# Kernel tuning notes

Hardware: AMD Instinct MI355X
Metric: run time of the kernel (lower is better)

## Reference

```python
import jax, jax.numpy as jnp
import numpy as np

N_EMBD = 1024
N_HEAD = 16
LORA_R = 8
LORA_ALPHA = 16
SCALE = LORA_ALPHA / LORA_R


def lora_linear(x, W, b, A, Bm):
    # loralib: F.linear(x, W, b) + (x @ A.T @ B.T) * scaling
    return x @ W.T + b + ((x @ A.T) @ Bm.T) * SCALE


def setup_inputs() -> dict:
    key = jax.random.key(0)
    ks = jax.random.split(key, 9)
    B, T, C = 4, 2048, N_EMBD
    s_in = 1.0 / np.sqrt(C)
    x = jax.random.normal(ks[0], (B, T, C), dtype=jnp.float32)
    Wqkv = jax.random.normal(ks[1], (3 * C, C), dtype=jnp.float32) * s_in
    bqkv = jnp.zeros((3 * C,), dtype=jnp.float32)
    Aqkv = jax.random.normal(ks[2], (LORA_R, C), dtype=jnp.float32) * s_in
    Bqkv = jnp.zeros((3 * C, LORA_R), dtype=jnp.float32)  # loralib inits B to zero
    Wproj = jax.random.normal(ks[3], (C, C), dtype=jnp.float32) * s_in
    bproj = jnp.zeros((C,), dtype=jnp.float32)
    Aproj = jax.random.normal(ks[4], (LORA_R, C), dtype=jnp.float32) * s_in
    Bproj = jnp.zeros((C, LORA_R), dtype=jnp.float32)
    return {"x": x, "Wqkv": Wqkv, "bqkv": bqkv, "Aqkv": Aqkv, "Bqkv": Bqkv,
            "Wproj": Wproj, "bproj": bproj, "Aproj": Aproj, "Bproj": Bproj}


def reference(x, Wqkv, bqkv, Aqkv, Bqkv, Wproj, bproj, Aproj, Bproj):
    B, T, C = x.shape
    H, D = N_HEAD, C // N_HEAD
    qkv = lora_linear(x, Wqkv, bqkv, Aqkv, Bqkv)  # [B,T,3C]
    q, k, v = jnp.split(qkv, 3, axis=2)
    # [B,T,C] -> [B,H,T,D]
    q = q.reshape(B, T, H, D).transpose(0, 2, 1, 3)
    k = k.reshape(B, T, H, D).transpose(0, 2, 1, 3)
    v = v.reshape(B, T, H, D).transpose(0, 2, 1, 3)
    att = jnp.einsum("bhqd,bhkd->bhqk", q, k) * (1.0 / np.sqrt(D))
    causal = jnp.tril(jnp.ones((T, T), dtype=bool))
    att = jnp.where(causal[None, None], att, jnp.float32(-jnp.inf))
    att = jax.nn.softmax(att, axis=-1)
    out = jnp.einsum("bhqk,bhkd->bhqd", att, v)  # [B,H,T,D]
    out = out.transpose(0, 2, 1, 3).reshape(B, T, C)
    return lora_linear(out, Wproj, bproj, Aproj, Bproj)
```

## Files before the change

### kernel.cpp

```cpp
#include <hip/hip_runtime.h>
#include <hip/hip_bf16.h>

typedef __bf16 bf16_t;
typedef __bf16 bf16x8 __attribute__((ext_vector_type(8)));
typedef __bf16 bf16x4 __attribute__((ext_vector_type(4)));
typedef float  f32x4  __attribute__((ext_vector_type(4)));

#define MFMA_BF16 __builtin_amdgcn_mfma_f32_16x16x32_bf16
#define NEG_BIG  (-3.0e38f)

#if __has_builtin(__builtin_amdgcn_exp2f)
#define EXP2F(x) __builtin_amdgcn_exp2f(x)
#else
#define EXP2F(x) exp2f(x)
#endif

#define SBAR()       __builtin_amdgcn_s_barrier()
#define SCHED0()     __builtin_amdgcn_sched_barrier(0)
#define WAIT_LGKM0() asm volatile("s_waitcnt lgkmcnt(0)" ::: "memory")
#define WAIT_LGKM8() asm volatile("s_waitcnt lgkmcnt(8)" ::: "memory")
#define WAIT_VM0()   asm volatile("s_waitcnt vmcnt(0)" ::: "memory")
#define WAIT_VM4()   asm volatile("s_waitcnt vmcnt(4)" ::: "memory")
#define WAIT_VM6()   asm volatile("s_waitcnt vmcnt(6)" ::: "memory")

__device__ __forceinline__ void load16_lds(const bf16_t* g, bf16_t* l) {
    __builtin_amdgcn_global_load_lds(
        (const __attribute__((address_space(1))) void*)g,
        (__attribute__((address_space(3))) void*)l, 16, 0, 0);
}

__device__ inline bf16x8 ld8(const bf16_t* p) { return *(const bf16x8*)p; }
__device__ inline bf16x8 ld8(const float* p) {
    f32x4 a = *(const f32x4*)p;
    f32x4 b = *(const f32x4*)(p + 4);
    bf16x8 o;
    o[0] = (bf16_t)a[0]; o[1] = (bf16_t)a[1]; o[2] = (bf16_t)a[2]; o[3] = (bf16_t)a[3];
    o[4] = (bf16_t)b[0]; o[5] = (bf16_t)b[1]; o[6] = (bf16_t)b[2]; o[7] = (bf16_t)b[3];
    return o;
}

template <typename TX>
__device__ __forceinline__ void lora_xa_body(
    const TX* __restrict__ X, const float* __restrict__ A,
    float* __restrict__ out, int m, int lane)
{
    const TX* xp = X + (size_t)m * 1024;
    float acc[8];
#pragma unroll
    for (int r = 0; r < 8; r++) acc[r] = 0.f;

#pragma unroll 4
    for (int ci = 0; ci < 16; ci++) {
        int k = ci * 64 + lane;
        float xv = (float)xp[k];
#pragma unroll
        for (int r = 0; r < 8; r++) acc[r] += xv * A[r * 1024 + k];
    }
#pragma unroll
    for (int r = 0; r < 8; r++) {
        float v = acc[r];
        v += __shfl_xor(v, 1);  v += __shfl_xor(v, 2);  v += __shfl_xor(v, 4);
        v += __shfl_xor(v, 8);  v += __shfl_xor(v, 16); v += __shfl_xor(v, 32);
        if (lane == 0) out[m * 8 + r] = v;
    }
}

template <typename TX>
__global__ __launch_bounds__(256) void lora_xa_kernel(
    const TX* __restrict__ X, const float* __restrict__ A,
    float* __restrict__ out)
{
    const int lane = threadIdx.x & 63;
    const int w    = threadIdx.x >> 6;
    const int m    = blockIdx.x * 4 + w;
    lora_xa_body<TX>(X, A, out, m, lane);
}

__global__ __launch_bounds__(256) void prep_kernel(
    const float* __restrict__ x, const float* __restrict__ Wqkv,
    const float* __restrict__ Wproj,
    bf16_t* __restrict__ x16, bf16_t* __restrict__ Wqkv16,
    bf16_t* __restrict__ Wproj16,
    const float* __restrict__ Aqkv, float* __restrict__ xa1)
{
    const int bid = blockIdx.x;
    if (bid < 6144) {
        const float* in; bf16_t* out; size_t off;
        if (bid < 4096)      { in = x;     out = x16;     off = (size_t)bid * 2048; }
        else if (bid < 5632) { in = Wqkv;  out = Wqkv16;  off = (size_t)(bid - 4096) * 2048; }
        else                 { in = Wproj; out = Wproj16; off = (size_t)(bid - 5632) * 2048; }
        size_t i = off + (size_t)threadIdx.x * 8;
        *(bf16x8*)&out[i] = ld8(&in[i]);
    } else {
        const int lane = threadIdx.x & 63;
        const int w    = threadIdx.x >> 6;
        const int m    = (bid - 6144) * 4 + w;
        lora_xa_body<float>(x, Aqkv, xa1, m, lane);
    }
}

__device__ __forceinline__ void gemm_epilogue(
    f32x4 (&acc)[4][4], const float* bias, const float* xA, const float* LB,
    bf16_t* C0, bf16_t* C1, bf16_t* C2, float* Cf,
    int tile_m, int tile_n, int wm, int wn, int c, int g)
{
    const int seg    = tile_n >> 10;
    const int tn_loc = tile_n & 1023;
    bf16_t* Cout = (seg == 0) ? C0 : (seg == 1) ? C1 : C2;

    float biasf[4];
    float lbv[4][8];
#pragma unroll
    for (int j = 0; j < 4; j++) {
        int col = tile_n + wn + j * 16 + c;
        biasf[j] = bias[col];
        f32x4 lb0 = *(const f32x4*)&LB[(size_t)col * 8];
        f32x4 lb1 = *(const f32x4*)&LB[(size_t)col * 8 + 4];
#pragma unroll
        for (int r = 0; r < 4; r++) { lbv[j][r] = lb0[r]; lbv[j][r + 4] = lb1[r]; }
    }
#pragma unroll
    for (int i = 0; i < 4; i++) {
#pragma unroll
        for (int rg = 0; rg < 4; rg++) {
            int row = tile_m + wm + i * 16 + g * 4 + rg;
            f32x4 xa0 = *(const f32x4*)&xA[(size_t)row * 8];
            f32x4 xa1 = *(const f32x4*)&xA[(size_t)row * 8 + 4];
#pragma unroll
            for (int j = 0; j < 4; j++) {
                float lora = xa0[0] * lbv[j][0] + xa0[1] * lbv[j][1] +
                             xa0[2] * lbv[j][2] + xa0[3] * lbv[j][3] +
                             xa1[0] * lbv[j][4] + xa1[1] * lbv[j][5] +
                             xa1[2] * lbv[j][6] + xa1[3] * lbv[j][7];
                float v = acc[i][j][rg] + biasf[j] + 2.0f * lora;
                int lcol = tn_loc + wn + j * 16 + c;
                if (Cf) Cf[(size_t)row * 1024 + lcol] = v;
                else    Cout[(size_t)row * 1024 + lcol] = (bf16_t)v;
            }
        }
    }
}

template <typename TA, typename TW>
__global__ __launch_bounds__(256) void gemm_bias_lora(
    const TA* __restrict__ A, const TW* __restrict__ W,
    const float* __restrict__ bias, const float* __restrict__ xA,
    const float* __restrict__ LB,
    bf16_t* __restrict__ C0, bf16_t* __restrict__ C1, bf16_t* __restrict__ C2,
    float* __restrict__ Cf, int K)
{
    __shared__ __align__(16) bf16_t As[128 * 72];
    __shared__ __align__(16) bf16_t Bs[128 * 72];

    const int t    = threadIdx.x;
    const int lane = t & 63;
    const int w    = t >> 6;
    const int wm   = (w >> 1) * 64;
    const int wn   = (w & 1) * 64;
    const int c    = lane & 15;
    const int g    = lane >> 4;
    const int tile_m = blockIdx.y * 128;
    const int tile_n = blockIdx.x * 128;

    const int srow = t >> 3;
    const int scol = (t & 7) * 8;

    f32x4 acc[4][4];
#pragma unroll
    for (int i = 0; i < 4; i++)
#pragma unroll
        for (int j = 0; j < 4; j++) {
            f32x4 z = {0.f, 0.f, 0.f, 0.f};
            acc[i][j] = z;
        }

    for (int k0 = 0; k0 < K; k0 += 64) {
#pragma unroll
        for (int i = 0; i < 4; i++) {
            int r = srow + i * 32;
            *(bf16x8*)&As[r * 72 + scol] = ld8(&A[(size_t)(tile_m + r) * K + k0 + scol]);
            *(bf16x8*)&Bs[r * 72 + scol] = ld8(&W[(size_t)(tile_n + r) * K + k0 + scol]);
        }
        __syncthreads();

#pragma unroll
        for (int kk = 0; kk < 2; kk++) {
            bf16x8 af[4], bfr[4];
#pragma unroll
            for (int i = 0; i < 4; i++)
                af[i] = *(const bf16x8*)&As[(wm + i * 16 + c) * 72 + kk * 32 + g * 8];
#pragma unroll
            for (int j = 0; j < 4; j++)
                bfr[j] = *(const bf16x8*)&Bs[(wn + j * 16 + c) * 72 + kk * 32 + g * 8];
#pragma unroll
            for (int i = 0; i < 4; i++)
#pragma unroll
                for (int j = 0; j < 4; j++)
                    acc[i][j] = MFMA_BF16(af[i], bfr[j], acc[i][j], 0, 0, 0);
        }
        __syncthreads();
    }
    gemm_epilogue(acc, bias, xA, LB, C0, C1, C2, Cf, tile_m, tile_n, wm, wn, c, g);
}

#define AS_OFF(row, q) ((row) * 64 + (((q) ^ ((row) & 7)) * 8))

__global__ __launch_bounds__(256) void gemm_async(
    const bf16_t* __restrict__ A, const bf16_t* __restrict__ W,
    const float* __restrict__ bias, const float* __restrict__ xA,
    const float* __restrict__ LB,
    bf16_t* __restrict__ C0, bf16_t* __restrict__ C1, bf16_t* __restrict__ C2,
    float* __restrict__ Cf, int K)
{
    __shared__ __align__(16) bf16_t As[128 * 64];
    __shared__ __align__(16) bf16_t Bs[128 * 64];

    const int t    = threadIdx.x;
    const int lane = t & 63;
    const int w    = t >> 6;
    const int wm   = (w >> 1) * 64;
    const int wn   = (w & 1) * 64;
    const int c    = lane & 15;
    const int g    = lane >> 4;
    const int tile_m = blockIdx.y * 128;
    const int tile_n = blockIdx.x * 128;

    const int trow = t >> 3;
    const int k8   = (t & 7) ^ (trow & 7);
    const bf16_t* Ab = A + (size_t)tile_m * K + k8 * 8;
    const bf16_t* Wb = W + (size_t)tile_n * K + k8 * 8;

    f32x4 acc[4][4];
#pragma unroll
    for (int i = 0; i < 4; i++)
#pragma unroll
        for (int j = 0; j < 4; j++) {
            f32x4 z = {0.f, 0.f, 0.f, 0.f};
            acc[i][j] = z;
        }

    for (int k0 = 0; k0 < K; k0 += 64) {
#pragma unroll
        for (int i = 0; i < 4; i++) {
            int row = i * 32 + trow;
            load16_lds(&Ab[(size_t)row * K + k0], &As[(i * 256 + t) * 8]);
            load16_lds(&Wb[(size_t)row * K + k0], &Bs[(i * 256 + t) * 8]);
        }
        __syncthreads();

#pragma unroll
        for (int kk = 0; kk < 2; kk++) {
            bf16x8 af[4], bfr[4];
#pragma unroll
            for (int i = 0; i < 4; i++)
                af[i] = *(const bf16x8*)&As[AS_OFF(wm + i * 16 + c, kk * 4 + g)];
#pragma unroll
            for (int j = 0; j < 4; j++)
                bfr[j] = *(const bf16x8*)&Bs[AS_OFF(wn + j * 16 + c, kk * 4 + g)];
#pragma unroll
            for (int i = 0; i < 4; i++)
#pragma unroll
                for (int j = 0; j < 4; j++)
                    acc[i][j] = MFMA_BF16(af[i], bfr[j], acc[i][j], 0, 0, 0);
        }
        __syncthreads();
    }
    gemm_epilogue(acc, bias, xA, LB, C0, C1, C2, Cf, tile_m, tile_n, wm, wn, c, g);
}

__global__ __launch_bounds__(512, 2) void gemm_256(
    const bf16_t* __restrict__ A, const bf16_t* __restrict__ W,
    const float* __restrict__ bias, const float* __restrict__ xA,
    const float* __restrict__ LB,
    bf16_t* __restrict__ C0, bf16_t* __restrict__ C1, bf16_t* __restrict__ C2,
    float* __restrict__ Cf, int K, int ntn)
{
    __shared__ __align__(16) bf16_t As[4][8192];
    __shared__ __align__(16) bf16_t Bs[4][8192];

    const int t    = threadIdx.x;
    const int lane = t & 63;
    const int w    = t >> 6;
    const int c    = lane & 15;
    const int g    = lane >> 4;

    const int nwg = gridDim.x;
    const int cpx = nwg >> 3;
    const int bid = blockIdx.x;
    const int swz = (bid & 7) * cpx + (bid >> 3);
    const int tile_m = (swz / ntn) * 256;
    const int tile_n = (swz % ntn) * 256;

    const int wm  = (w >> 2) * 128;
    const int wn  = (w & 3) * 64;
    const int ha  = w >> 2;
    const int hb  = wn >> 7;
    const int wnl = wn & 127;

    int aoffs[8][2], boffs[4][2];
#pragma unroll
    for (int il = 0; il < 8; il++) {
        int rl = il * 16 + c;
#pragma unroll
        for (int ks = 0; ks < 2; ks++)
            aoffs[il][ks] = rl * 64 + (((ks * 4 + g) ^ (rl & 7)) * 8);
    }
#pragma unroll
    for (int j2 = 0; j2 < 4; j2++) {
        int rl = wnl + j2 * 16 + c;
#pragma unroll
        for (int ks = 0; ks < 2; ks++)
            boffs[j2][ks] = rl * 64 + (((ks * 4 + g) ^ (rl & 7)) * 8);
    }

    const int trow = t >> 3;
    const int qq   = (t & 7) ^ (trow & 7);
    const bf16_t* aO = A + (size_t)(tile_m + trow) * K + qq * 8;
    const bf16_t* wO = W + (size_t)(tile_n + trow) * K + qq * 8;
    const size_t rK64 = (size_t)64 * K;

#define STAGE_A(T, h) do {                                                         \
    load16_lds(aO + (size_t)(h) * 128 * K + (size_t)(T) * 64,                      \
               &As[((T) & 1) * 2 + (h)][t * 8]);                                   \
    load16_lds(aO + (size_t)(h) * 128 * K + rK64 + (size_t)(T) * 64,               \
               &As[((T) & 1) * 2 + (h)][4096 + t * 8]); } while (0)
#define STAGE_B(T, h) do {                                                         \
    load16_lds(wO + (size_t)(h) * 128 * K + (size_t)(T) * 64,                      \
               &Bs[((T) & 1) * 2 + (h)][t * 8]);                                   \
    load16_lds(wO + (size_t)(h) * 128 * K + rK64 + (size_t)(T) * 64,               \
               &Bs[((T) & 1) * 2 + (h)][4096 + t * 8]); } while (0)

    f32x4 acc[8][4];
#pragma unroll
    for (int i = 0; i < 8; i++)
#pragma unroll
        for (int j2 = 0; j2 < 4; j2++) {
            f32x4 z = {0.f, 0.f, 0.f, 0.f};
            acc[i][j2] = z;
        }

    const int NT = K >> 6;

    STAGE_B(0, 0); STAGE_B(0, 1); STAGE_A(0, 0); STAGE_A(0, 1);
    WAIT_VM4();
    STAGE_B(1, 0); STAGE_B(1, 1); STAGE_A(1, 0);
    WAIT_VM6();
    SBAR();

    for (int j = 0; j < NT; j++) {
        const bf16_t* Ab = &As[(j & 1) * 2 + ha][0];
        const bf16_t* Bb = &Bs[(j & 1) * 2 + hb][0];
        bf16x8 bfr[4][2], af0[4], af1[4];

#pragma unroll
        for (int j2 = 0; j2 < 4; j2++) {
            bfr[j2][0] = *(const bf16x8*)&Bb[boffs[j2][0]];
            bfr[j2][1] = *(const bf16x8*)&Bb[boffs[j2][1]];
        }
#pragma unroll
        for (int i = 0; i < 4; i++) af0[i] = *(const bf16x8*)&Ab[aoffs[i][0]];
        if (j + 1 < NT) STAGE_A(j + 1, 1);
        WAIT_LGKM8();
        SBAR();
        WAIT_LGKM0();
        SCHED0();
        __builtin_amdgcn_s_setprio(1);
#pragma unroll
        for (int i = 0; i < 4; i++)
#pragma unroll
            for (int j2 = 0; j2 < 4; j2++)
                acc[i][j2] = MFMA_BF16(af0[i], bfr[j2][0], acc[i][j2], 0, 0, 0);
        __builtin_amdgcn_s_setprio(0);
        SBAR();

#pragma unroll
        for (int i = 0; i < 4; i++) af1[i] = *(const bf16x8*)&Ab[aoffs[i + 4][0]];
        if (j + 2 < NT) STAGE_B(j + 2, 0);
        SBAR();
        WAIT_LGKM0();
        SCHED0();
        __builtin_amdgcn_s_setprio(1);
#pragma unroll
        for (int i = 0; i < 4; i++)
#pragma unroll
            for (int j2 = 0; j2 < 4; j2++)
                acc[4 + i][j2] = MFMA_BF16(af1[i], bfr[j2][0], acc[4 + i][j2], 0, 0, 0);
        __builtin_amdgcn_s_setprio(0);
        SBAR();

#pragma unroll
        for (int i = 0; i < 4; i++) af0[i] = *(const bf16x8*)&Ab[aoffs[i][1]];
#pragma unroll
        for (int i = 0; i < 4; i++) af1[i] = *(const bf16x8*)&Ab[aoffs[i + 4][1]];
        if (j + 2 < NT) STAGE_B(j + 2, 1);
        SBAR();
        WAIT_LGKM0();
        SCHED0();
        __builtin_amdgcn_s_setprio(1);
#pragma unroll
        for (int i = 0; i < 4; i++)
#pragma unroll
            for (int j2 = 0; j2 < 4; j2++)
                acc[i][j2] = MFMA_BF16(af0[i], bfr[j2][1], acc[i][j2], 0, 0, 0);
        __builtin_amdgcn_s_setprio(0);
        SBAR();

        if (j + 2 < NT) STAGE_A(j + 2, 0);
        SBAR();
        __builtin_amdgcn_s_setprio(1);
#pragma unroll
        for (int i = 0; i < 4; i++)
#pragma unroll
            for (int j2 = 0; j2 < 4; j2++)
                acc[4 + i][j2] = MFMA_BF16(af1[i], bfr[j2][1], acc[4 + i][j2], 0, 0, 0);
        __builtin_amdgcn_s_setprio(0);
        if (j < NT - 2) WAIT_VM6(); else WAIT_VM0();
        SBAR();
    }
#undef STAGE_A
#undef STAGE_B

    const int seg    = tile_n >> 10;
    const int tn_loc = tile_n & 1023;
    bf16_t* Cout = (seg == 0) ? C0 : (seg == 1) ? C1 : C2;

    float biasf[4];
    float lbv[4][8];
#pragma unroll
    for (int j2 = 0; j2 < 4; j2++) {
        int col = tile_n + wn + j2 * 16 + c;
        biasf[j2] = bias[col];
        f32x4 lb0 = *(const f32x4*)&LB[(size_t)col * 8];
        f32x4 lb1 = *(const f32x4*)&LB[(size_t)col * 8 + 4];
#pragma unroll
        for (int r = 0; r < 4; r++) { lbv[j2][r] = lb0[r]; lbv[j2][r + 4] = lb1[r]; }
    }
#pragma unroll
    for (int i = 0; i < 8; i++) {
#pragma unroll
        for (int rg = 0; rg < 4; rg++) {
            int row = tile_m + wm + i * 16 + g * 4 + rg;
            f32x4 xa0 = *(const f32x4*)&xA[(size_t)row * 8];
            f32x4 xa1 = *(const f32x4*)&xA[(size_t)row * 8 + 4];
#pragma unroll
            for (int j2 = 0; j2 < 4; j2++) {
                float lora = xa0[0] * lbv[j2][0] + xa0[1] * lbv[j2][1] +
                             xa0[2] * lbv[j2][2] + xa0[3] * lbv[j2][3] +
                             xa1[0] * lbv[j2][4] + xa1[1] * lbv[j2][5] +
                             xa1[2] * lbv[j2][6] + xa1[3] * lbv[j2][7];
                float v = acc[i][j2][rg] + biasf[j2] + 2.0f * lora;
                int lcol = tn_loc + wn + j2 * 16 + c;
                if (Cf) Cf[(size_t)row * 1024 + lcol] = v;
                else    Cout[(size_t)row * 1024 + lcol] = (bf16_t)v;
            }
        }
    }
}

#define VT_IDX(d, kv) ((d) * 72 + ((d) >> 4) * 16 + (kv))
#define PS_IDX(q, kv) ((q) * 72 + ((q) >> 2) * 8 + (kv))
#define PW_REGION 1168

__global__ __launch_bounds__(256, 2) void attn_kernel(
    bf16_t* __restrict__ Q, const bf16_t* __restrict__ Kg,
    const bf16_t* __restrict__ Vg)
{
    __shared__ __align__(16) bf16_t Ks[64 * 72];
    __shared__ __align__(16) bf16_t Vt[64 * 72 + 64];
    __shared__ __align__(16) bf16_t Ps[8 * PW_REGION];

    const int t    = threadIdx.x;
    const int lane = t & 63;
    const int w    = t >> 6;
    const int c    = lane & 15;
    const int g    = lane >> 4;

    const int id = blockIdx.x;
    const int qb = 15 - (id >> 6);
    const int h  = id & 15;
    const int b  = (id >> 4) & 3;
    const int q0 = qb * 128;
    const size_t base = (size_t)b * 2048 * 1024;
    const int last = 2 * qb + 1;

    bf16x8 qfA[2], qfB[2];
    {
        const bf16_t* qpA = Q + base + (size_t)(q0 + w * 16 + c) * 1024 + h * 64;
        qfA[0] = *(const bf16x8*)&qpA[g * 8];
        qfA[1] = *(const bf16x8*)&qpA[32 + g * 8];
        const bf16_t* qpB = qpA + (size_t)64 * 1024;
        qfB[0] = *(const bf16x8*)&qpB[g * 8];
        qfB[1] = *(const bf16x8*)&qpB[32 + g * 8];
    }

    bf16x8 ones;
#pragma unroll
    for (int e = 0; e < 8; e++) ones[e] = (bf16_t)1.0f;

    f32x4 accA[4], accB[4];
#pragma unroll
    for (int jd = 0; jd < 4; jd++) {
        f32x4 z = {0.f, 0.f, 0.f, 0.f};
        accA[jd] = z; accB[jd] = z;
    }
    f32x4 lA = {0.f, 0.f, 0.f, 0.f};
    f32x4 lB = {0.f, 0.f, 0.f, 0.f};
    float mA = NEG_BIG, mB = NEG_BIG;

    const int sr = t >> 2;
    const int sc = (t & 3) * 16;
    const int vtbase = VT_IDX(sc, sr);

    bf16x8 kr0, kr1, vr0, vr1;
    {
        const bf16_t* kp = Kg + base + (size_t)sr * 1024 + h * 64 + sc;
        kr0 = *(const bf16x8*)&kp[0];
        kr1 = *(const bf16x8*)&kp[8];
        const bf16_t* vp = Vg + base + (size_t)sr * 1024 + h * 64 + sc;
        vr0 = *(const bf16x8*)&vp[0];
        vr1 = *(const bf16x8*)&vp[8];
    }

    bf16_t* PwA = &Ps[(w * 2 + 0) * PW_REGION];
    bf16_t* PwB = &Ps[(w * 2 + 1) * PW_REGION];
    const float SCL = 0.125f * 1.44269504088896f;

    for (int kt = 0; kt <= last; kt++) {
        if (kt > 0) __syncthreads();
        *(bf16x8*)&Ks[sr * 72 + sc]     = kr0;
        *(bf16x8*)&Ks[sr * 72 + sc + 8] = kr1;
#pragma unroll
        for (int e = 0; e < 8; e++) Vt[vtbase + e * 72]       = vr0[e];
#pragma unroll
        for (int e = 0; e < 8; e++) Vt[vtbase + (e + 8) * 72] = vr1[e];
        __syncthreads();

        if (kt < last) {
            const bf16_t* kp = Kg + base + (size_t)((kt + 1) * 64 + sr) * 1024 + h * 64 + sc;
            kr0 = *(const bf16x8*)&kp[0];
            kr1 = *(const bf16x8*)&kp[8];
            const bf16_t* vp = Vg + base + (size_t)((kt + 1) * 64 + sr) * 1024 + h * 64 + sc;
            vr0 = *(const bf16x8*)&vp[0];
            vr1 = *(const bf16x8*)&vp[8];
        }

        const bool doA = (kt <= 2 * qb);

        f32x4 sA[4], sB[4];
#pragma unroll
        for (int j = 0; j < 4; j++) {
            f32x4 z = {0.f, 0.f, 0.f, 0.f};
            sA[j] = z; sB[j] = z;
        }
#pragma unroll
        for (int kk = 0; kk < 2; kk++) {
            bf16x8 kf[4];
#pragma unroll
            for (int j = 0; j < 4; j++)
                kf[j] = *(const bf16x8*)&Ks[(j * 16 + c) * 72 + kk * 32 + g * 8];
            if (doA) {
#pragma unroll
                for (int j = 0; j < 4; j++)
                    sA[j] = MFMA_BF16(kf[j], qfA[kk], sA[j], 0, 0, 0);
            }
#pragma unroll
            for (int j = 0; j < 4; j++)
                sB[j] = MFMA_BF16(kf[j], qfB[kk], sB[j], 0, 0, 0);
        }

        if (doA) {
#pragma unroll
            for (int j = 0; j < 4; j++)
#pragma unroll
                for (int r = 0; r < 4; r++) sA[j][r] *= SCL;
            if (kt == 2 * qb) {
#pragma unroll
                for (int j = 0; j < 4; j++)
#pragma unroll
                    for (int r = 0; r < 4; r++)
                        if (j * 16 + g * 4 + r > w * 16 + c) sA[j][r] = NEG_BIG;
            }
            float mx;
            {
                float a0 = fmaxf(fmaxf(sA[0][0], sA[0][1]), fmaxf(sA[0][2], sA[0][3]));
                float a1 = fmaxf(fmaxf(sA[1][0], sA[1][1]), fmaxf(sA[1][2], sA[1][3]));
                float a2 = fmaxf(fmaxf(sA[2][0], sA[2][1]), fmaxf(sA[2][2], sA[2][3]));
                float a3 = fmaxf(fmaxf(sA[3][0], sA[3][1]), fmaxf(sA[3][2], sA[3][3]));
                mx = fmaxf(fmaxf(a0, a1), fmaxf(a2, a3));
                mx = fmaxf(mx, __shfl_xor(mx, 16));
                mx = fmaxf(mx, __shfl_xor(mx, 32));
            }
            if (!__all(mx <= mA + 8.0f)) {
                float mnew  = fmaxf(mA, mx);
                float alpha = EXP2F(mA - mnew);
                mA = mnew;
#pragma unroll
                for (int jd = 0; jd < 4; jd++)
#pragma unroll
                    for (int r = 0; r < 4; r++) accA[jd][r] *= alpha;
                lA[0] *= alpha;
            }
#pragma unroll
            for (int j = 0; j < 4; j++)
#pragma unroll
                for (int r = 0; r < 4; r++) sA[j][r] = EXP2F(sA[j][r] - mA);
#pragma unroll
            for (int j = 0; j < 4; j++) {
                bf16x4 pk;
#pragma unroll
                for (int r = 0; r < 4; r++) pk[r] = (bf16_t)sA[j][r];
                *(bf16x4*)&PwA[PS_IDX(c, j * 16 + g * 4)] = pk;
            }
        }

        {
#pragma unroll
            for (int j = 0; j < 4; j++)
#pragma unroll
                for (int r = 0; r < 4; r++) sB[j][r] *= SCL;
            if (kt == last) {
#pragma unroll
                for (int j = 0; j < 4; j++)
#pragma unroll
                    for (int r = 0; r < 4; r++)
                        if (j * 16 + g * 4 + r > w * 16 + c) sB[j][r] = NEG_BIG;
            }
            float mx;
            {
                float a0 = fmaxf(fmaxf(sB[0][0], sB[0][1]), fmaxf(sB[0][2], sB[0][3]));
                float a1 = fmaxf(fmaxf(sB[1][0], sB[1][1]), fmaxf(sB[1][2], sB[1][3]));
                float a2 = fmaxf(fmaxf(sB[2][0], sB[2][1]), fmaxf(sB[2][2], sB[2][3]));
                float a3 = fmaxf(fmaxf(sB[3][0], sB[3][1]), fmaxf(sB[3][2], sB[3][3]));
                mx = fmaxf(fmaxf(a0, a1), fmaxf(a2, a3));
                mx = fmaxf(mx, __shfl_xor(mx, 16));
                mx = fmaxf(mx, __shfl_xor(mx, 32));
            }
            if (!__all(mx <= mB + 8.0f)) {
                float mnew  = fmaxf(mB, mx);
                float alpha = EXP2F(mB - mnew);
                mB = mnew;
#pragma unroll
                for (int jd = 0; jd < 4; jd++)
#pragma unroll
                    for (int r = 0; r < 4; r++) accB[jd][r] *= alpha;
                lB[0] *= alpha;
            }
#pragma unroll
            for (int j = 0; j < 4; j++)
#pragma unroll
                for (int r = 0; r < 4; r++) sB[j][r] = EXP2F(sB[j][r] - mB);
#pragma unroll
            for (int j = 0; j < 4; j++) {
                bf16x4 pk;
#pragma unroll
                for (int r = 0; r < 4; r++) pk[r] = (bf16_t)sB[j][r];
                *(bf16x4*)&PwB[PS_IDX(c, j * 16 + g * 4)] = pk;
            }
        }

#pragma unroll
        for (int kkv = 0; kkv < 2; kkv++) {
            bf16x8 vf[4];
#pragma unroll
            for (int jd = 0; jd < 4; jd++)
                vf[jd] = *(const bf16x8*)&Vt[VT_IDX(jd * 16 + c, kkv * 32 + g * 8)];
            if (doA) {
                bf16x8 pfA = *(const bf16x8*)&PwA[PS_IDX(c, kkv * 32 + g * 8)];
#pragma unroll
                for (int jd = 0; jd < 4; jd++)
                    accA[jd] = MFMA_BF16(vf[jd], pfA, accA[jd], 0, 0, 0);
                lA = MFMA_BF16(ones, pfA, lA, 0, 0, 0);
            }
            bf16x8 pfB = *(const bf16x8*)&PwB[PS_IDX(c, kkv * 32 + g * 8)];
#pragma unroll
            for (int jd = 0; jd < 4; jd++)
                accB[jd] = MFMA_BF16(vf[jd], pfB, accB[jd], 0, 0, 0);
            lB = MFMA_BF16(ones, pfB, lB, 0, 0, 0);
        }
    }

    {
        float rl = 1.0f / lA[0];
        bf16_t* op = Q + base + (size_t)(q0 + w * 16 + c) * 1024 + h * 64;
#pragma unroll
        for (int jd = 0; jd < 4; jd++) {
            bf16x4 o4;
#pragma unroll
            for (int r = 0; r < 4; r++) o4[r] = (bf16_t)(accA[jd][r] * rl);
            *(bf16x4*)&op[jd * 16 + g * 4] = o4;
        }
    }
    {
        float rl = 1.0f / lB[0];
        bf16_t* op = Q + base + (size_t)(q0 + 64 + w * 16 + c) * 1024 + h * 64;
#pragma unroll
        for (int jd = 0; jd < 4; jd++) {
            bf16x4 o4;
#pragma unroll
            for (int r = 0; r < 4; r++) o4[r] = (bf16_t)(accB[jd][r] * rl);
            *(bf16x4*)&op[jd * 16 + g * 4] = o4;
        }
    }
}

extern "C" void kernel_launch(void* const* d_in, const int* in_sizes, int n_in,
                              void* d_out, int out_size, void* d_ws, size_t ws_size,
                              hipStream_t stream) {
    const float* x     = (const float*)d_in[0];
    const float* Wqkv  = (const float*)d_in[1];
    const float* bqkv  = (const float*)d_in[2];
    const float* Aqkv  = (const float*)d_in[3];
    const float* Bqkv  = (const float*)d_in[4];
    const float* Wproj = (const float*)d_in[5];
    const float* bproj = (const float*)d_in[6];
    const float* Aproj = (const float*)d_in[7];
    const float* Bproj = (const float*)d_in[8];
    float* out = (float*)d_out;

    char* ws = (char*)d_ws;
    const bool big = ws_size >= (size_t)(72.5 * 1024 * 1024) + 65536;

    if (big) {
        float*  xa1    = (float*)ws;
        float*  xa2    = (float*)(ws + 262144);
        bf16_t* x16    = (bf16_t*)(ws + 524288);
        bf16_t* Wqkv16 = x16 + (size_t)8192 * 1024;
        bf16_t* Wproj16= Wqkv16 + (size_t)3072 * 1024;
        bf16_t* Qfull  = Wproj16 + (size_t)1024 * 1024;
        bf16_t* Kfull  = Qfull + (size_t)8192 * 1024;
        bf16_t* Vfull  = Kfull + (size_t)8192 * 1024;

        prep_kernel<<<8192, 256, 0, stream>>>(
            x, Wqkv, Wproj, x16, Wqkv16, Wproj16, Aqkv, xa1);

        gemm_256<<<384, 512, 0, stream>>>(
            x16, Wqkv16, bqkv, xa1, Bqkv, Qfull, Kfull, Vfull, nullptr, 1024, 12);

        attn_kernel<<<1024, 256, 0, stream>>>(Qfull, Kfull, Vfull);

        lora_xa_kernel<bf16_t><<<2048, 256, 0, stream>>>(Qfull, Aproj, xa2);

        gemm_async<<<dim3(8, 64), 256, 0, stream>>>(
            Qfull, Wproj16, bproj, xa2, Bproj,
            nullptr, nullptr, nullptr, out, 1024);
    } else {
        float*  xa1   = (float*)ws;
        float*  xa2   = (float*)(ws + 262144);
        bf16_t* Qfull = (bf16_t*)(ws + 524288);
        bf16_t* Kfull = Qfull + (size_t)8192 * 1024;
        bf16_t* Vfull = Kfull + (size_t)8192 * 1024;

        lora_xa_kernel<float><<<2048, 256, 0, stream>>>(x, Aqkv, xa1);
        gemm_bias_lora<float, float><<<dim3(24, 64), 256, 0, stream>>>(
            x, Wqkv, bqkv, xa1, Bqkv, Qfull, Kfull, Vfull, nullptr, 1024);
        attn_kernel<<<1024, 256, 0, stream>>>(Qfull, Kfull, Vfull);
        lora_xa_kernel<bf16_t><<<2048, 256, 0, stream>>>(Qfull, Aproj, xa2);
        gemm_bias_lora<bf16_t, float><<<dim3(8, 64), 256, 0, stream>>>(
            Qfull, Wproj, bproj, xa2, Bproj,
            nullptr, nullptr, nullptr, out, 1024);
    }
}
```

Measured before the change: 315.9 us.

## Fuse LoRA down-projection into output projection GEMM via extra MFMAs

Drops the separate lora_xa_kernel before the output projection. Each block of the projection GEMM now converts Aproj to bf16 in shared memory and computes x·Aᵀ for its 128 rows with extra MFMAs on the A tiles already staged in LDS. The rank-8 LoRA up-projection is then applied in a custom epilogue. This removes one launch and a pass over the attention output, but every one of the 8 column blocks recomputes the same xA. It also adds about 16KB of shared memory per block and computes xA in bf16 rather than fp32.

```diff
diff --git a/kernel.cpp b/kernel.cpp
--- a/kernel.cpp
+++ b/kernel.cpp
@@ -205,15 +205,14 @@
 
 #define AS_OFF(row, q) ((row) * 64 + (((q) ^ ((row) & 7)) * 8))
 
-__global__ __launch_bounds__(256) void gemm_async(
+__global__ __launch_bounds__(256) void gemm_proj_fused(
     const bf16_t* __restrict__ A, const bf16_t* __restrict__ W,
-    const float* __restrict__ bias, const float* __restrict__ xA,
-    const float* __restrict__ LB,
-    bf16_t* __restrict__ C0, bf16_t* __restrict__ C1, bf16_t* __restrict__ C2,
-    float* __restrict__ Cf, int K)
+    const float* __restrict__ bias, const float* __restrict__ Ap,
+    const float* __restrict__ LB, float* __restrict__ Cf, int K)
 {
     __shared__ __align__(16) bf16_t As[128 * 64];
     __shared__ __align__(16) bf16_t Bs[128 * 64];
+    __shared__ __align__(16) bf16_t Ap16[8 * 1032];
 
     const int t    = threadIdx.x;
     const int lane = t & 63;
@@ -225,6 +224,16 @@
     const int tile_m = blockIdx.y * 128;
     const int tile_n = blockIdx.x * 128;
 
+    {
+        int r = t >> 5;
+        int k = (t & 31) * 32;
+        const float* src = Ap + (size_t)r * 1024 + k;
+        bf16_t* dst = &Ap16[r * 1032 + k];
+#pragma unroll
+        for (int e = 0; e < 32; e += 8)
+            *(bf16x8*)&dst[e] = ld8(&src[e]);
+    }
+
     const int trow = t >> 3;
     const int k8   = (t & 7) ^ (trow & 7);
     const bf16_t* Ab = A + (size_t)tile_m * K + k8 * 8;
@@ -238,6 +247,11 @@
             f32x4 z = {0.f, 0.f, 0.f, 0.f};
             acc[i][j] = z;
         }
+    f32x4 accx[2];
+    {
+        f32x4 z = {0.f, 0.f, 0.f, 0.f};
+        accx[0] = z; accx[1] = z;
+    }
 
     for (int k0 = 0; k0 < K; k0 += 64) {
 #pragma unroll
@@ -262,10 +276,56 @@
 #pragma unroll
                 for (int j = 0; j < 4; j++)
                     acc[i][j] = MFMA_BF16(af[i], bfr[j], acc[i][j], 0, 0, 0);
+            bf16x8 apf = *(const bf16x8*)&Ap16[(c & 7) * 1032 + k0 + kk * 32 + g * 8];
+#pragma unroll
+            for (int fi = 0; fi < 2; fi++) {
+                bf16x8 xf = *(const bf16x8*)&As[AS_OFF(w * 32 + fi * 16 + c, kk * 4 + g)];
+                accx[fi] = MFMA_BF16(xf, apf, accx[fi], 0, 0, 0);
+            }
         }
         __syncthreads();
     }
-    gemm_epilogue(acc, bias, xA, LB, C0, C1, C2, Cf, tile_m, tile_n, wm, wn, c, g);
+
+    float* xa2l = (float*)As;
+    if (c < 8) {
+#pragma unroll
+        for (int fi = 0; fi < 2; fi++)
+#pragma unroll
+            for (int rg = 0; rg < 4; rg++)
+                xa2l[(w * 32 + fi * 16 + g * 4 + rg) * 8 + c] = accx[fi][rg];
+    }
+    __syncthreads();
+
+    float biasf[4];
+    float lbv[4][8];
+#pragma unroll
+    for (int j = 0; j < 4; j++) {
+        int col = tile_n + wn + j * 16 + c;
+        biasf[j] = bias[col];
+        f32x4 lb0 = *(const f32x4*)&LB[(size_t)col * 8];
+        f32x4 lb1 = *(const f32x4*)&LB[(size_t)col * 8 + 4];
+#pragma unroll
+        for (int r = 0; r < 4; r++) { lbv[j][r] = lb0[r]; lbv[j][r + 4] = lb1[r]; }
+    }
+#pragma unroll
+    for (int i = 0; i < 4; i++) {
+#pragma unroll
+        for (int rg = 0; rg < 4; rg++) {
+            int rloc = wm + i * 16 + g * 4 + rg;
+            int row  = tile_m + rloc;
+            f32x4 xa0 = *(const f32x4*)&xa2l[rloc * 8];
+            f32x4 xa1 = *(const f32x4*)&xa2l[rloc * 8 + 4];
+#pragma unroll
+            for (int j = 0; j < 4; j++) {
+                float lora = xa0[0] * lbv[j][0] + xa0[1] * lbv[j][1] +
+                             xa0[2] * lbv[j][2] + xa0[3] * lbv[j][3] +
+                             xa1[0] * lbv[j][4] + xa1[1] * lbv[j][5] +
+                             xa1[2] * lbv[j][6] + xa1[3] * lbv[j][7];
+                float v = acc[i][j][rg] + biasf[j] + 2.0f * lora;
+                Cf[(size_t)row * 1024 + tile_n + wn + j * 16 + c] = v;
+            }
+        }
+    }
 }
 
 __global__ __launch_bounds__(512, 2) void gemm_256(
@@ -722,7 +782,6 @@
 
     if (big) {
         float*  xa1    = (float*)ws;
-        float*  xa2    = (float*)(ws + 262144);
         bf16_t* x16    = (bf16_t*)(ws + 524288);
         bf16_t* Wqkv16 = x16 + (size_t)8192 * 1024;
         bf16_t* Wproj16= Wqkv16 + (size_t)3072 * 1024;
@@ -738,11 +797,8 @@
 
         attn_kernel<<<1024, 256, 0, stream>>>(Qfull, Kfull, Vfull);
 
-        lora_xa_kernel<bf16_t><<<2048, 256, 0, stream>>>(Qfull, Aproj, xa2);
-
-        gemm_async<<<dim3(8, 64), 256, 0, stream>>>(
-            Qfull, Wproj16, bproj, xa2, Bproj,
-            nullptr, nullptr, nullptr, out, 1024);
+        gemm_proj_fused<<<dim3(8, 64), 256, 0, stream>>>(
+            Qfull, Wproj16, bproj, Aproj, Bproj, out, 1024);
     } else {
         float*  xa1   = (float*)ws;
         float*  xa2   = (float*)(ws + 262144);
```

After: 301.1 us. -4.7%, faster.
